# Kernel optimization log

Measured on AMD Instinct MI355X. Metric: run time of the kernel, lower is better.

## Reference

```python
import jax, jax.numpy as jnp
import numpy as np

N = 20000   # nodes
E = 640000  # edges (avg degree 32)
D = 128     # input_nf == output_nf
H = 128     # hidden_size


def silu(x):
    return x * jax.nn.sigmoid(x)


def setup_inputs() -> dict:
    key = jax.random.key(0)
    ks = jax.random.split(key, 16)
    def lin(k, out_d, in_d, scale=None):
        s = scale if scale is not None else (1.0 / np.sqrt(in_d))
        return jax.random.uniform(k, (out_d, in_d), jnp.float32, -s, s)
    return {
        "h": jax.random.normal(ks[0], (N, D), jnp.float32),
        "coord": jax.random.normal(ks[1], (N, 3), jnp.float32),
        "edge_index": jax.random.randint(ks[2], (2, E), 0, N, jnp.int32),
        # edge_mlp: Linear(2D+1 -> H), Linear(H -> H)
        "We1": lin(ks[3], H, 2 * D + 1), "be1": jnp.zeros((H,), jnp.float32),
        "We2": lin(ks[4], H, H),          "be2": jnp.zeros((H,), jnp.float32),
        # node_mlp: Linear(H+D -> H), Linear(H -> D)
        "Wn1": lin(ks[5], H, H + D),      "bn1": jnp.zeros((H,), jnp.float32),
        "Wn2": lin(ks[6], D, H),          "bn2": jnp.zeros((D,), jnp.float32),
        # coord_mlp: Linear(H -> H), Linear(H -> 1, no bias, xavier gain=0.001)
        "Wc1": lin(ks[7], H, H),          "bc1": jnp.zeros((H,), jnp.float32),
        "Wc2": lin(ks[8], 1, H, scale=0.001 * np.sqrt(6.0 / (H + 1))),
    }


def reference(h, coord, edge_index, We1, be1, We2, be2, Wn1, bn1, Wn2, bn2, Wc1, bc1, Wc2):
    src, dst = edge_index[0], edge_index[1]

    # coord2radial (normalize=False)
    coord_diff = coord[src] - coord[dst]                 # [E, 3]
    radial = jnp.sum(coord_diff * coord_diff, axis=1, keepdims=True)  # [E, 1]

    # edge model: cat(h[src], h[dst], radial) -> Lin -> SiLU -> Lin -> SiLU
    e_in = jnp.concatenate([h[src], h[dst], radial], axis=1)  # [E, 2D+1]
    edge_feat = silu(silu(e_in @ We1.T + be1) @ We2.T + be2)  # [E, H]

    # coord model: coord_diff * coord_mlp(edge_feat), scatter-add over src
    w = silu(edge_feat @ Wc1.T + bc1) @ Wc2.T                 # [E, 1]
    trans = coord_diff * w                                    # [E, 3]
    coord_out = coord + jax.ops.segment_sum(trans, src, num_segments=N)

    # node model: agg edge_feat over src, cat(h, agg) -> Lin -> SiLU -> Lin, residual
    agg = jax.ops.segment_sum(edge_feat, src, num_segments=N)  # [N, H]
    n_in = jnp.concatenate([h, agg], axis=1)                   # [N, H+D]
    h_out = h + (silu(n_in @ Wn1.T + bn1) @ Wn2.T + bn2)       # [N, D]

    return (h_out, coord_out)
```

## Files before the change

kernel.cpp:

```cpp
#include <hip/hip_runtime.h>

#define N_NODES 20000
#define N_EDGES 640000
#define D 128
#define H 128

#define EB    128
#define TPB   512
#define NBLK2 512
#define NTILE (N_EDGES / EB)
#define EBN   64
#define NNT64 ((N_NODES + EBN - 1) / EBN)
#define ST    136

#define WS_W1   0
#define WS_W2   65536
#define WS_WC1  98304
#define WS_WN1  131072
#define WS_WN2  196608
#define WS_CNT  229376
#define WS_CUR  309376
#define WS_PERM 389376
#define WS_U    2949376
#define WS_V    8069376
#define WS_P    13189376

typedef short bf16x8 __attribute__((ext_vector_type(8)));
typedef float f32x4  __attribute__((ext_vector_type(4)));

__device__ __forceinline__ float silu_f(float x) {
    return x * __builtin_amdgcn_rcpf(1.0f + __expf(-x));
}
__device__ __forceinline__ ushort f2b(float f) {
    union { float f; unsigned int u; } v; v.f = f;
    return (ushort)((v.u + 0x7FFF + ((v.u >> 16) & 1)) >> 16);
}
__device__ __forceinline__ float b2f(ushort s) {
    union { unsigned int u; float f; } v; v.u = ((unsigned int)s) << 16; return v.f;
}
__device__ __forceinline__ unsigned f2b2(float lo, float hi) {
    unsigned r;
    asm("v_cvt_pk_bf16_f32 %0, %1, %2" : "=v"(r) : "v"(lo), "v"(hi));
    return r;
}

__device__ __forceinline__ void bar_lds() {
    asm volatile("s_waitcnt lgkmcnt(0)" ::: "memory");
    __builtin_amdgcn_s_barrier();
    asm volatile("" ::: "memory");
}

__device__ __forceinline__ void gemm_chunk_rw(const ushort* Ab, int kc0,
                                              const bf16x8 b[2], f32x4 acc[4][2],
                                              int eg, int lane)
{
    const int r = lane & 15, g = lane >> 4;
    bf16x8 a[4];
    #pragma unroll
    for (int mt = 0; mt < 4; ++mt)
        a[mt] = *(const bf16x8*)&Ab[(eg * 64 + mt * 16 + r) * ST + kc0 + g * 8];
    #pragma unroll
    for (int mt = 0; mt < 4; ++mt)
        #pragma unroll
        for (int nt = 0; nt < 2; ++nt)
            acc[mt][nt] = __builtin_amdgcn_mfma_f32_16x16x32_bf16(a[mt], b[nt], acc[mt][nt], 0, 0, 0);
}

__device__ __forceinline__ void zero_acc8(f32x4 acc[4][2]) {
    #pragma unroll
    for (int mt = 0; mt < 4; ++mt)
        #pragma unroll
        for (int nt = 0; nt < 2; ++nt)
            acc[mt][nt] = (f32x4){0.f, 0.f, 0.f, 0.f};
}

__device__ __forceinline__ void epi_silu8(f32x4 acc[4][2], const float* bias,
                                          ushort* out, int eg, int cg, int lane) {
    const int r = lane & 15, g = lane >> 4;
    #pragma unroll
    for (int nt = 0; nt < 2; ++nt) {
        int o = cg * 32 + nt * 16 + r;
        float bo = bias[o];
        #pragma unroll
        for (int mt = 0; mt < 4; ++mt)
            #pragma unroll
            for (int j = 0; j < 4; ++j) {
                int e = eg * 64 + mt * 16 + g * 4 + j;
                out[e * ST + o] = f2b(silu_f(acc[mt][nt][j] + bo));
            }
    }
}

__device__ __forceinline__ void epi_silu8_pk(f32x4 acc[4][2], const float* bias,
                                             ushort* out, int eg, int cg, int lane) {
    const int r = lane & 15, g = lane >> 4;
    #pragma unroll
    for (int nt = 0; nt < 2; ++nt) {
        int o = cg * 32 + nt * 16 + r;
        float bo = bias[o];
        #pragma unroll
        for (int mt = 0; mt < 4; ++mt) {
            int e = eg * 64 + mt * 16 + g * 4;
            unsigned p01 = f2b2(silu_f(acc[mt][nt][0] + bo), silu_f(acc[mt][nt][1] + bo));
            unsigned p23 = f2b2(silu_f(acc[mt][nt][2] + bo), silu_f(acc[mt][nt][3] + bo));
            out[(e + 0) * ST + o] = (ushort)p01;
            out[(e + 1) * ST + o] = (ushort)(p01 >> 16);
            out[(e + 2) * ST + o] = (ushort)p23;
            out[(e + 3) * ST + o] = (ushort)(p23 >> 16);
        }
    }
}

__global__ void prep2(const float* __restrict__ We1, const float* __restrict__ We2,
                      const float* __restrict__ Wc1, const float* __restrict__ Wn1,
                      const float* __restrict__ Wn2, const float* __restrict__ coordp,
                      const int* __restrict__ eidx,
                      ushort* w1, ushort* w2, ushort* wc1, ushort* wn1, ushort* wn2,
                      float* cout, int* cnt)
{
    int idx = blockIdx.x * 256 + threadIdx.x;
    if (idx < N_EDGES) atomicAdd(&cnt[eidx[idx]], 1);
    int j = idx;
    if (j < 32768) { w1[j] = f2b(We1[(j >> 8) * 257 + (j & 255)]); return; }
    j -= 32768;
    if (j < 16384) { w2[j] = f2b(We2[j]); return; }
    j -= 16384;
    if (j < 16384) { wc1[j] = f2b(Wc1[j]); return; }
    j -= 16384;
    if (j < 32768) { wn1[j] = f2b(Wn1[j]); return; }
    j -= 32768;
    if (j < 16384) { wn2[j] = f2b(Wn2[j]); return; }
    j -= 16384;
    if (j < N_NODES * 3) cout[j] = coordp[j];
}

__global__ __launch_bounds__(256, 2)
void uvp_k(const float* __restrict__ h,
           const ushort* __restrict__ w1b, const ushort* __restrict__ wn1b,
           const float* __restrict__ be1, const float* __restrict__ bn1,
           ushort* __restrict__ u, ushort* __restrict__ v, ushort* __restrict__ p)
{
    __shared__ __align__(16) ushort hs[EBN * ST];
    __shared__ float b1s[H], bn1s[H];

    const int tid = threadIdx.x, lane = tid & 63, wv = tid >> 6;
    const int eg = wv >> 2, cg = wv & 3;
    const int r = lane & 15, g = lane >> 4;
    const int n0 = blockIdx.x * EBN;

    if (tid < 128) b1s[tid] = be1[tid];
    else if (tid < 256) bn1s[tid - 128] = bn1[tid - 128];

    bf16x8 wa[4][2], wb[4][2], wn[4][2];
    {
        const int c0 = cg * 32 + r, c1c = c0 + 16;
        #pragma unroll
        for (int kc = 0; kc < 4; ++kc) {
            wa[kc][0] = *(const bf16x8*)&w1b [c0  * 256 +       kc * 32 + g * 8];
            wa[kc][1] = *(const bf16x8*)&w1b [c1c * 256 +       kc * 32 + g * 8];
            wb[kc][0] = *(const bf16x8*)&w1b [c0  * 256 + 128 + kc * 32 + g * 8];
            wb[kc][1] = *(const bf16x8*)&w1b [c1c * 256 + 128 + kc * 32 + g * 8];
            wn[kc][0] = *(const bf16x8*)&wn1b[c0  * 256 +       kc * 32 + g * 8];
            wn[kc][1] = *(const bf16x8*)&wn1b[c1c * 256 +       kc * 32 + g * 8];
        }
    }
    #pragma unroll
    for (int it = 0; it < 8; ++it) {
        int idx = tid + it * 256;
        int e = idx >> 5, c = idx & 31;
        int n = n0 + e; if (n >= N_NODES) n = 0;
        float4 vv = *(const float4*)&h[(size_t)n * D + c * 4];
        ushort4 pk; pk.x = f2b(vv.x); pk.y = f2b(vv.y); pk.z = f2b(vv.z); pk.w = f2b(vv.w);
        *(ushort4*)&hs[e * ST + c * 4] = pk;
    }
    __syncthreads();

    f32x4 acc[4][2];
    zero_acc8(acc);
    #pragma unroll
    for (int kc = 0; kc < 4; ++kc) gemm_chunk_rw(hs, kc * 32, wa[kc], acc, eg, lane);
    #pragma unroll
    for (int nt = 0; nt < 2; ++nt) {
        int o = cg * 32 + nt * 16 + r;
        float bo = b1s[o];
        #pragma unroll
        for (int mt = 0; mt < 4; ++mt)
            #pragma unroll
            for (int j = 0; j < 4; ++j) {
                int n = n0 + eg * 64 + mt * 16 + g * 4 + j;
                if (n < N_NODES) u[(size_t)n * H + o] = f2b(acc[mt][nt][j] + bo);
            }
    }
    zero_acc8(acc);
    #pragma unroll
    for (int kc = 0; kc < 4; ++kc) gemm_chunk_rw(hs, kc * 32, wb[kc], acc, eg, lane);
    #pragma unroll
    for (int nt = 0; nt < 2; ++nt) {
        int o = cg * 32 + nt * 16 + r;
        #pragma unroll
        for (int mt = 0; mt < 4; ++mt)
            #pragma unroll
            for (int j = 0; j < 4; ++j) {
                int n = n0 + eg * 64 + mt * 16 + g * 4 + j;
                if (n < N_NODES) v[(size_t)n * H + o] = f2b(acc[mt][nt][j]);
            }
    }
    zero_acc8(acc);
    #pragma unroll
    for (int kc = 0; kc < 4; ++kc) gemm_chunk_rw(hs, kc * 32, wn[kc], acc, eg, lane);
    #pragma unroll
    for (int nt = 0; nt < 2; ++nt) {
        int o = cg * 32 + nt * 16 + r;
        float bo = bn1s[o];
        #pragma unroll
        for (int mt = 0; mt < 4; ++mt)
            #pragma unroll
            for (int j = 0; j < 4; ++j) {
                int n = n0 + eg * 64 + mt * 16 + g * 4 + j;
                if (n < N_NODES) p[(size_t)n * H + o] = f2b(acc[mt][nt][j] + bo);
            }
    }
}

__global__ void scan_k(const int* __restrict__ cnt, int* cur) {
    __shared__ int wsum[16];
    __shared__ int carry_s;
    const int t = threadIdx.x, lane = t & 63, wid = t >> 6;
    if (t == 0) carry_s = 0;
    __syncthreads();
    for (int base = 0; base < N_NODES; base += 1024) {
        int i = base + t;
        int vv = (i < N_NODES) ? cnt[i] : 0;
        int s = vv;
        #pragma unroll
        for (int d = 1; d < 64; d <<= 1) {
            int x = __shfl_up(s, d);
            if (lane >= d) s += x;
        }
        if (lane == 63) wsum[wid] = s;
        __syncthreads();
        if (wid == 0) {
            int ws = (lane < 16) ? wsum[lane] : 0;
            #pragma unroll
            for (int d = 1; d < 16; d <<= 1) {
                int x = __shfl_up(ws, d);
                if (lane >= d) ws += x;
            }
            if (lane < 16) wsum[lane] = ws;
        }
        __syncthreads();
        int woff = (wid > 0) ? wsum[wid - 1] : 0;
        if (i < N_NODES) cur[i] = carry_s + woff + s - vv;
        __syncthreads();
        if (t == 0) carry_s += wsum[15];
        __syncthreads();
    }
}

__global__ void scatter_k(const int* __restrict__ eidx, int* cur, int* perm) {
    int e = blockIdx.x * 256 + threadIdx.x;
    if (e < N_EDGES) {
        int pp = atomicAdd(&cur[eidx[e]], 1);
        perm[pp] = e;
    }
}

__global__ __launch_bounds__(TPB, 2)
void egcl_edge(const ushort* __restrict__ u, const ushort* __restrict__ v,
               const int* __restrict__ eidx, const int* __restrict__ perm,
               const float* __restrict__ coordp,
               const ushort* __restrict__ w2b, const ushort* __restrict__ wc1b,
               const float* __restrict__ We1,
               const float* __restrict__ be2, const float* __restrict__ bc1,
               const float* __restrict__ Wc2,
               float* __restrict__ agg, float* __restrict__ coord_out)
{
    __shared__ __align__(16) ushort t1[EB * ST];
    __shared__ __align__(16) ushort ef[EB * ST];
    __shared__ int   srcs_s[2][EB], dsts_s[2][EB];
    __shared__ float radial_s[2][EB];
    __shared__ float cdx_s[2][EB], cdy_s[2][EB], cdz_s[2][EB];
    __shared__ float wcop[4][EB];
    __shared__ float b2s[H], bc1s[H], wc2s[H], w256s[H];

    const int tid = threadIdx.x, lane = tid & 63, wv = tid >> 6;
    const int eg = wv >> 2, cg = wv & 3;
    const int r = lane & 15, g = lane >> 4;
    const int ce = tid >> 2, cq = tid & 3;

    if (tid < 128)      b2s[tid] = be2[tid];
    else if (tid < 256) bc1s[tid - 128] = bc1[tid - 128];
    else if (tid < 384) wc2s[tid - 256] = Wc2[tid - 256];
    else                w256s[tid - 384] = We1[(tid - 384) * 257 + 256];

    bf16x8 w2f[4][2], w3f[4][2];
    {
        const int c0 = cg * 32 + r, c1c = c0 + 16;
        #pragma unroll
        for (int kc = 0; kc < 4; ++kc) {
            w2f[kc][0] = *(const bf16x8*)&w2b [c0  * 128 + kc * 32 + g * 8];
            w2f[kc][1] = *(const bf16x8*)&w2b [c1c * 128 + kc * 32 + g * 8];
            w3f[kc][0] = *(const bf16x8*)&wc1b[c0  * 128 + kc * 32 + g * 8];
            w3f[kc][1] = *(const bf16x8*)&wc1b[c1c * 128 + kc * 32 + g * 8];
        }
    }

    int t = (int)blockIdx.x;
    int rs = 0, rd = 0;
    float rsx = 0, rsy = 0, rsz = 0, rdx = 0, rdy = 0, rdz = 0;
    if (tid < EB) {
        int e = perm[t * EB + tid];
        int s = eidx[e], d = eidx[N_EDGES + e];
        srcs_s[0][tid] = s; dsts_s[0][tid] = d;
        float sx = coordp[s * 3], sy = coordp[s * 3 + 1], sz = coordp[s * 3 + 2];
        float dx0 = coordp[d * 3], dy0 = coordp[d * 3 + 1], dz0 = coordp[d * 3 + 2];
        float dx = sx - dx0, dy = sy - dy0, dz = sz - dz0;
        cdx_s[0][tid] = dx; cdy_s[0][tid] = dy; cdz_s[0][tid] = dz;
        radial_s[0][tid] = dx * dx + dy * dy + dz * dz;
    }
    __syncthreads();

    bf16x8 uvr[8];
    {
        const ushort* up = u + (size_t)srcs_s[0][ce] * H + cq * 32;
        const ushort* vp = v + (size_t)dsts_s[0][ce] * H + cq * 32;
        #pragma unroll
        for (int i = 0; i < 4; ++i) {
            uvr[i]     = *(const bf16x8*)(up + i * 8);
            uvr[4 + i] = *(const bf16x8*)(vp + i * 8);
        }
    }
    if (tid < EB && t + NBLK2 < NTILE) {
        int e = perm[(t + NBLK2) * EB + tid];
        rs = eidx[e]; rd = eidx[N_EDGES + e];
        rsx = coordp[rs * 3]; rsy = coordp[rs * 3 + 1]; rsz = coordp[rs * 3 + 2];
        rdx = coordp[rd * 3]; rdy = coordp[rd * 3 + 1]; rdz = coordp[rd * 3 + 2];
    }

    f32x4 acc[4][2];
    int pb = 0;

    for (; t < NTILE; t += NBLK2) {
        {
            float rad = radial_s[pb][ce];
            #pragma unroll
            for (int i = 0; i < 4; ++i) {
                float4 wlo = *(const float4*)&w256s[cq * 32 + i * 8];
                float4 whi = *(const float4*)&w256s[cq * 32 + i * 8 + 4];
                bf16x8 uu = uvr[i], vx = uvr[4 + i];
                float x0 = silu_f(b2f((ushort)uu[0]) + b2f((ushort)vx[0]) + rad * wlo.x);
                float x1 = silu_f(b2f((ushort)uu[1]) + b2f((ushort)vx[1]) + rad * wlo.y);
                float x2 = silu_f(b2f((ushort)uu[2]) + b2f((ushort)vx[2]) + rad * wlo.z);
                float x3 = silu_f(b2f((ushort)uu[3]) + b2f((ushort)vx[3]) + rad * wlo.w);
                float x4 = silu_f(b2f((ushort)uu[4]) + b2f((ushort)vx[4]) + rad * whi.x);
                float x5 = silu_f(b2f((ushort)uu[5]) + b2f((ushort)vx[5]) + rad * whi.y);
                float x6 = silu_f(b2f((ushort)uu[6]) + b2f((ushort)vx[6]) + rad * whi.z);
                float x7 = silu_f(b2f((ushort)uu[7]) + b2f((ushort)vx[7]) + rad * whi.w);
                uint4 pk4;
                pk4.x = f2b2(x0, x1); pk4.y = f2b2(x2, x3);
                pk4.z = f2b2(x4, x5); pk4.w = f2b2(x6, x7);
                *(uint4*)&t1[ce * ST + cq * 32 + i * 8] = pk4;
            }
        }
        if (tid < EB) {
            srcs_s[pb ^ 1][tid] = rs; dsts_s[pb ^ 1][tid] = rd;
            float dx = rsx - rdx, dy = rsy - rdy, dz = rsz - rdz;
            cdx_s[pb ^ 1][tid] = dx; cdy_s[pb ^ 1][tid] = dy; cdz_s[pb ^ 1][tid] = dz;
            radial_s[pb ^ 1][tid] = dx * dx + dy * dy + dz * dz;
        }
        bar_lds();

        int en = 0;
        if (tid < EB && t + 2 * NBLK2 < NTILE) en = perm[(t + 2 * NBLK2) * EB + tid];
        zero_acc8(acc);
        __builtin_amdgcn_s_setprio(1);
        #pragma unroll
        for (int kc = 0; kc < 4; ++kc) gemm_chunk_rw(t1, kc * 32, w2f[kc], acc, eg, lane);
        __builtin_amdgcn_s_setprio(0);
        epi_silu8_pk(acc, b2s, ef, eg, cg, lane);
        bar_lds();

        {
            const ushort* up = u + (size_t)srcs_s[pb ^ 1][ce] * H + cq * 32;
            const ushort* vp = v + (size_t)dsts_s[pb ^ 1][ce] * H + cq * 32;
            #pragma unroll
            for (int i = 0; i < 4; ++i) {
                uvr[i]     = *(const bf16x8*)(up + i * 8);
                uvr[4 + i] = *(const bf16x8*)(vp + i * 8);
            }
        }
        int rs2 = 0, rd2 = 0;
        if (tid < EB) { rs2 = eidx[en]; rd2 = eidx[N_EDGES + en]; }
        {
            f32x4 acc3[2][4];
            #pragma unroll
            for (int ot = 0; ot < 2; ++ot)
                #pragma unroll
                for (int et = 0; et < 4; ++et)
                    acc3[ot][et] = (f32x4){0.f, 0.f, 0.f, 0.f};
            __builtin_amdgcn_s_setprio(1);
            #pragma unroll
            for (int kc = 0; kc < 4; ++kc) {
                bf16x8 bfr[4];
                #pragma unroll
                for (int et = 0; et < 4; ++et)
                    bfr[et] = *(const bf16x8*)&ef[(eg * 64 + et * 16 + r) * ST + kc * 32 + g * 8];
                #pragma unroll
                for (int ot = 0; ot < 2; ++ot)
                    #pragma unroll
                    for (int et = 0; et < 4; ++et)
                        acc3[ot][et] = __builtin_amdgcn_mfma_f32_16x16x32_bf16(
                            w3f[kc][ot], bfr[et], acc3[ot][et], 0, 0, 0);
            }
            __builtin_amdgcn_s_setprio(0);
            float partial[4] = {0.f, 0.f, 0.f, 0.f};
            #pragma unroll
            for (int ot = 0; ot < 2; ++ot) {
                int ob = cg * 32 + ot * 16 + g * 4;
                float4 wq = *(const float4*)&wc2s[ob];
                float4 bq = *(const float4*)&bc1s[ob];
                #pragma unroll
                for (int et = 0; et < 4; ++et) {
                    partial[et] += silu_f(acc3[ot][et][0] + bq.x) * wq.x
                                 + silu_f(acc3[ot][et][1] + bq.y) * wq.y
                                 + silu_f(acc3[ot][et][2] + bq.z) * wq.z
                                 + silu_f(acc3[ot][et][3] + bq.w) * wq.w;
                }
            }
            #pragma unroll
            for (int et = 0; et < 4; ++et) {
                float s_ = partial[et];
                s_ += __shfl_xor(s_, 16);
                s_ += __shfl_xor(s_, 32);
                if (g == 0) wcop[cg][eg * 64 + et * 16 + r] = s_;
            }
        }
        {
            int o = tid & 127, q = tid >> 7;
            int base = q * 32;
            float sum = 0.f;
            int curs = srcs_s[pb][base];
            for (int k = 0; k < 32; ++k) {
                int e = base + k;
                int s = srcs_s[pb][e];
                if (s != curs) {
                    atomicAdd(&agg[(size_t)curs * D + o], sum);
                    sum = 0.f; curs = s;
                }
                sum += b2f(ef[e * ST + o]);
            }
            atomicAdd(&agg[(size_t)curs * D + o], sum);
        }
        bar_lds();

        if (tid < EB) {
            rs = rs2; rd = rd2;
            rsx = coordp[rs * 3]; rsy = coordp[rs * 3 + 1]; rsz = coordp[rs * 3 + 2];
            rdx = coordp[rd * 3]; rdy = coordp[rd * 3 + 1]; rdz = coordp[rd * 3 + 2];
        }
        {
            float s_ = wcop[cq][ce];
            s_ += __shfl_down(s_, 2);
            s_ += __shfl_down(s_, 1);
            float wfull = __shfl(s_, lane & ~3);
            if (cq < 3) {
                float cdv = (cq == 0) ? cdx_s[pb][ce] : (cq == 1) ? cdy_s[pb][ce] : cdz_s[pb][ce];
                atomicAdd(&coord_out[(size_t)srcs_s[pb][ce] * 3 + cq], cdv * wfull);
            }
        }
        bar_lds();
        pb ^= 1;
    }
}

__global__ __launch_bounds__(256, 4)
void egcl_node(const float* __restrict__ h,
               const ushort* __restrict__ wn1b, const ushort* __restrict__ wn2b,
               const ushort* __restrict__ pArr, const float* __restrict__ bn2,
               float* __restrict__ hout )
{
    __shared__ __align__(16) ushort t1[EBN * ST];
    __shared__ __align__(16) ushort t2[EBN * ST];
    __shared__ float b2s[H];

    const int tid = threadIdx.x, lane = tid & 63, wv = tid >> 6;
    const int eg = wv >> 2, cg = wv & 3;
    const int r = lane & 15, g = lane >> 4;
    const int n0 = blockIdx.x * EBN;

    if (tid < 128) b2s[tid] = bn2[tid];

    bf16x8 wnb[4][2], w2f[4][2];
    {
        const int c0 = cg * 32 + r, c1c = c0 + 16;
        #pragma unroll
        for (int kc = 0; kc < 4; ++kc) {
            wnb[kc][0] = *(const bf16x8*)&wn1b[c0  * 256 + 128 + kc * 32 + g * 8];
            wnb[kc][1] = *(const bf16x8*)&wn1b[c1c * 256 + 128 + kc * 32 + g * 8];
            w2f[kc][0] = *(const bf16x8*)&wn2b[c0  * 128 + kc * 32 + g * 8];
            w2f[kc][1] = *(const bf16x8*)&wn2b[c1c * 128 + kc * 32 + g * 8];
        }
    }
    #pragma unroll
    for (int it = 0; it < 8; ++it) {
        int idx = tid + it * 256;
        int e = idx >> 5, c = idx & 31;
        int n = n0 + e; if (n >= N_NODES) n = 0;
        float4 vv = *(const float4*)&hout[(size_t)n * D + c * 4];
        ushort4 pk; pk.x = f2b(vv.x); pk.y = f2b(vv.y); pk.z = f2b(vv.z); pk.w = f2b(vv.w);
        *(ushort4*)&t1[e * ST + c * 4] = pk;
    }
    __syncthreads();

    f32x4 acc[4][2];
    zero_acc8(acc);
    #pragma unroll
    for (int kc = 0; kc < 4; ++kc) gemm_chunk_rw(t1, kc * 32, wnb[kc], acc, eg, lane);
    #pragma unroll
    for (int nt = 0; nt < 2; ++nt) {
        int o = cg * 32 + nt * 16 + r;
        #pragma unroll
        for (int mt = 0; mt < 4; ++mt)
            #pragma unroll
            for (int j = 0; j < 4; ++j) {
                int e = eg * 64 + mt * 16 + g * 4 + j;
                int n = n0 + e; if (n >= N_NODES) n = 0;
                float x = acc[mt][nt][j] + b2f(pArr[(size_t)n * H + o]);
                t2[e * ST + o] = f2b(silu_f(x));
            }
    }
    __syncthreads();

    zero_acc8(acc);
    #pragma unroll
    for (int kc = 0; kc < 4; ++kc) gemm_chunk_rw(t2, kc * 32, w2f[kc], acc, eg, lane);
    #pragma unroll
    for (int nt = 0; nt < 2; ++nt) {
        int o = cg * 32 + nt * 16 + r;
        float bo = b2s[o];
        #pragma unroll
        for (int mt = 0; mt < 4; ++mt)
            #pragma unroll
            for (int j = 0; j < 4; ++j) {
                int n = n0 + eg * 64 + mt * 16 + g * 4 + j;
                if (n < N_NODES)
                    hout[(size_t)n * D + o] = h[(size_t)n * D + o] + acc[mt][nt][j] + bo;
            }
    }
}

extern "C" void kernel_launch(void* const* d_in, const int* in_sizes, int n_in,
                              void* d_out, int out_size, void* d_ws, size_t ws_size,
                              hipStream_t stream)
{
    const float* h     = (const float*)d_in[0];
    const float* coord = (const float*)d_in[1];
    const int*   eidx  = (const int*)d_in[2];
    const float* We1 = (const float*)d_in[3];
    const float* be1 = (const float*)d_in[4];
    const float* We2 = (const float*)d_in[5];
    const float* be2 = (const float*)d_in[6];
    const float* Wn1 = (const float*)d_in[7];
    const float* bn1 = (const float*)d_in[8];
    const float* Wn2 = (const float*)d_in[9];
    const float* bn2 = (const float*)d_in[10];
    const float* Wc1 = (const float*)d_in[11];
    const float* bc1 = (const float*)d_in[12];
    const float* Wc2 = (const float*)d_in[13];

    float* hout = (float*)d_out;
    float* cout = (float*)d_out + (size_t)N_NODES * D;

    char* ws = (char*)d_ws;
    ushort* w1b  = (ushort*)(ws + WS_W1);
    ushort* w2b  = (ushort*)(ws + WS_W2);
    ushort* wc1b = (ushort*)(ws + WS_WC1);
    ushort* wn1b = (ushort*)(ws + WS_WN1);
    ushort* wn2b = (ushort*)(ws + WS_WN2);
    int* cnt  = (int*)(ws + WS_CNT);
    int* cur  = (int*)(ws + WS_CUR);
    int* perm = (int*)(ws + WS_PERM);
    ushort* uArr = (ushort*)(ws + WS_U);
    ushort* vArr = (ushort*)(ws + WS_V);
    ushort* pArr = (ushort*)(ws + WS_P);

    hipMemsetAsync(hout, 0, (size_t)N_NODES * D * sizeof(float), stream);
    hipMemsetAsync(cnt, 0, N_NODES * sizeof(int), stream);
    prep2<<<(N_EDGES + 255) / 256, 256, 0, stream>>>(We1, We2, Wc1, Wn1, Wn2, coord, eidx,
                                                     w1b, w2b, wc1b, wn1b, wn2b, cout, cnt);
    scan_k<<<1, 1024, 0, stream>>>(cnt, cur);
    scatter_k<<<(N_EDGES + 255) / 256, 256, 0, stream>>>(eidx, cur, perm);
    uvp_k<<<NNT64, 256, 0, stream>>>(h, w1b, wn1b, be1, bn1, uArr, vArr, pArr);
    egcl_edge<<<NBLK2, TPB, 0, stream>>>(uArr, vArr, eidx, perm, coord,
                                         w2b, wc1b, We1, be2, bc1, Wc2,
                                         hout, cout);
    egcl_node<<<NNT64, 256, 0, stream>>>(h, wn1b, wn2b, pArr, bn2, hout);
}
```

Before: 319.7 us.

## Fuse scan into prep via last-block pattern, merge scatter into uvp, drop barrier

The separate single-block scan kernel is folded into prep2: the last block to finish, detected by an atomic counter, does the prefix scan. The edge-permutation scatter becomes extra blocks of the uvp kernel, which removes two launches and their serialization. In egcl_edge, the per-edge coord weight is reduced with shuffles and atomically added straight to coord_out, so the wcop LDS buffer and one barrier per tile go away. In exchange, coord_out takes more atomics because each column group adds its own partial, and the serial scan now runs as the tail of prep2.

```diff
diff --git a/kernel.cpp b/kernel.cpp
--- a/kernel.cpp
+++ b/kernel.cpp
@@ -11,6 +11,7 @@
 #define NTILE (N_EDGES / EB)
 #define EBN   64
 #define NNT64 ((N_NODES + EBN - 1) / EBN)
+#define NSCAT ((N_EDGES + 255) / 256)
 #define ST    136
 
 #define WS_W1   0
@@ -111,39 +112,88 @@
     }
 }
 
-__global__ void prep2(const float* __restrict__ We1, const float* __restrict__ We2,
-                      const float* __restrict__ Wc1, const float* __restrict__ Wn1,
-                      const float* __restrict__ Wn2, const float* __restrict__ coordp,
-                      const int* __restrict__ eidx,
-                      ushort* w1, ushort* w2, ushort* wc1, ushort* wn1, ushort* wn2,
-                      float* cout, int* cnt)
+__global__ __launch_bounds__(1024)
+void prep2(const float* __restrict__ We1, const float* __restrict__ We2,
+           const float* __restrict__ Wc1, const float* __restrict__ Wn1,
+           const float* __restrict__ Wn2, const float* __restrict__ coordp,
+           const int* __restrict__ eidx,
+           ushort* w1, ushort* w2, ushort* wc1, ushort* wn1, ushort* wn2,
+           float* cout, int* cnt, int* cur)
 {
-    int idx = blockIdx.x * 256 + threadIdx.x;
+    const int tid = threadIdx.x;
+    int idx = blockIdx.x * 1024 + tid;
     if (idx < N_EDGES) atomicAdd(&cnt[eidx[idx]], 1);
     int j = idx;
-    if (j < 32768) { w1[j] = f2b(We1[(j >> 8) * 257 + (j & 255)]); return; }
-    j -= 32768;
-    if (j < 16384) { w2[j] = f2b(We2[j]); return; }
-    j -= 16384;
-    if (j < 16384) { wc1[j] = f2b(Wc1[j]); return; }
-    j -= 16384;
-    if (j < 32768) { wn1[j] = f2b(Wn1[j]); return; }
-    j -= 32768;
-    if (j < 16384) { wn2[j] = f2b(Wn2[j]); return; }
-    j -= 16384;
-    if (j < N_NODES * 3) cout[j] = coordp[j];
+    if (j < 32768) { w1[j] = f2b(We1[(j >> 8) * 257 + (j & 255)]); }
+    else if ((j -= 32768) < 16384) { w2[j] = f2b(We2[j]); }
+    else if ((j -= 16384) < 16384) { wc1[j] = f2b(Wc1[j]); }
+    else if ((j -= 16384) < 32768) { wn1[j] = f2b(Wn1[j]); }
+    else if ((j -= 32768) < 16384) { wn2[j] = f2b(Wn2[j]); }
+    else if ((j -= 16384) < N_NODES * 3) { cout[j] = coordp[j]; }
+
+    __shared__ int lastFlag;
+    __shared__ int wsum[16];
+    __shared__ int carry_s;
+    __threadfence();
+    __syncthreads();
+    if (tid == 0) lastFlag = (atomicAdd(&cnt[N_NODES], 1) == (int)gridDim.x - 1);
+    __syncthreads();
+    if (!lastFlag) return;
+    __threadfence();
+    const int lane = tid & 63, wid = tid >> 6;
+    if (tid == 0) carry_s = 0;
+    __syncthreads();
+    for (int base = 0; base < N_NODES; base += 1024) {
+        int i = base + tid;
+        int vv = 0;
+        if (i < N_NODES)
+            vv = __hip_atomic_load(&cnt[i], __ATOMIC_RELAXED, __HIP_MEMORY_SCOPE_AGENT);
+        int s = vv;
+        #pragma unroll
+        for (int d = 1; d < 64; d <<= 1) {
+            int x = __shfl_up(s, d);
+            if (lane >= d) s += x;
+        }
+        if (lane == 63) wsum[wid] = s;
+        __syncthreads();
+        if (wid == 0) {
+            int ws = (lane < 16) ? wsum[lane] : 0;
+            #pragma unroll
+            for (int d = 1; d < 16; d <<= 1) {
+                int x = __shfl_up(ws, d);
+                if (lane >= d) ws += x;
+            }
+            if (lane < 16) wsum[lane] = ws;
+        }
+        __syncthreads();
+        int woff = (wid > 0) ? wsum[wid - 1] : 0;
+        if (i < N_NODES) cur[i] = carry_s + woff + s - vv;
+        __syncthreads();
+        if (tid == 0) carry_s += wsum[15];
+        __syncthreads();
+    }
 }
 
 __global__ __launch_bounds__(256, 2)
-void uvp_k(const float* __restrict__ h,
-           const ushort* __restrict__ w1b, const ushort* __restrict__ wn1b,
-           const float* __restrict__ be1, const float* __restrict__ bn1,
-           ushort* __restrict__ u, ushort* __restrict__ v, ushort* __restrict__ p)
+void uvp_scatter_k(const float* __restrict__ h,
+                   const ushort* __restrict__ w1b, const ushort* __restrict__ wn1b,
+                   const float* __restrict__ be1, const float* __restrict__ bn1,
+                   ushort* __restrict__ u, ushort* __restrict__ v, ushort* __restrict__ p,
+                   const int* __restrict__ eidx, int* cur, int* perm)
 {
+    const int tid = threadIdx.x;
+    if (blockIdx.x >= NNT64) {
+        int e = (blockIdx.x - NNT64) * 256 + tid;
+        if (e < N_EDGES) {
+            int pp = atomicAdd(&cur[eidx[e]], 1);
+            perm[pp] = e;
+        }
+        return;
+    }
     __shared__ __align__(16) ushort hs[EBN * ST];
     __shared__ float b1s[H], bn1s[H];
 
-    const int tid = threadIdx.x, lane = tid & 63, wv = tid >> 6;
+    const int lane = tid & 63, wv = tid >> 6;
     const int eg = wv >> 2, cg = wv & 3;
     const int r = lane & 15, g = lane >> 4;
     const int n0 = blockIdx.x * EBN;
@@ -219,49 +269,6 @@
                 int n = n0 + eg * 64 + mt * 16 + g * 4 + j;
                 if (n < N_NODES) p[(size_t)n * H + o] = f2b(acc[mt][nt][j] + bo);
             }
-    }
-}
-
-__global__ void scan_k(const int* __restrict__ cnt, int* cur) {
-    __shared__ int wsum[16];
-    __shared__ int carry_s;
-    const int t = threadIdx.x, lane = t & 63, wid = t >> 6;
-    if (t == 0) carry_s = 0;
-    __syncthreads();
-    for (int base = 0; base < N_NODES; base += 1024) {
-        int i = base + t;
-        int vv = (i < N_NODES) ? cnt[i] : 0;
-        int s = vv;
-        #pragma unroll
-        for (int d = 1; d < 64; d <<= 1) {
-            int x = __shfl_up(s, d);
-            if (lane >= d) s += x;
-        }
-        if (lane == 63) wsum[wid] = s;
-        __syncthreads();
-        if (wid == 0) {
-            int ws = (lane < 16) ? wsum[lane] : 0;
-            #pragma unroll
-            for (int d = 1; d < 16; d <<= 1) {
-                int x = __shfl_up(ws, d);
-                if (lane >= d) ws += x;
-            }
-            if (lane < 16) wsum[lane] = ws;
-        }
-        __syncthreads();
-        int woff = (wid > 0) ? wsum[wid - 1] : 0;
-        if (i < N_NODES) cur[i] = carry_s + woff + s - vv;
-        __syncthreads();
-        if (t == 0) carry_s += wsum[15];
-        __syncthreads();
-    }
-}
-
-__global__ void scatter_k(const int* __restrict__ eidx, int* cur, int* perm) {
-    int e = blockIdx.x * 256 + threadIdx.x;
-    if (e < N_EDGES) {
-        int pp = atomicAdd(&cur[eidx[e]], 1);
-        perm[pp] = e;
     }
 }
 
@@ -280,7 +287,6 @@
     __shared__ int   srcs_s[2][EB], dsts_s[2][EB];
     __shared__ float radial_s[2][EB];
     __shared__ float cdx_s[2][EB], cdy_s[2][EB], cdz_s[2][EB];
-    __shared__ float wcop[4][EB];
     __shared__ float b2s[H], bc1s[H], wc2s[H], w256s[H];
 
     const int tid = threadIdx.x, lane = tid & 63, wv = tid >> 6;
@@ -427,13 +433,21 @@
                                  + silu_f(acc3[ot][et][3] + bq.w) * wq.w;
                 }
             }
+            const float* cdp = (g == 0) ? cdx_s[pb] : (g == 1) ? cdy_s[pb] : cdz_s[pb];
             #pragma unroll
             for (int et = 0; et < 4; ++et) {
                 float s_ = partial[et];
                 s_ += __shfl_xor(s_, 16);
                 s_ += __shfl_xor(s_, 32);
-                if (g == 0) wcop[cg][eg * 64 + et * 16 + r] = s_;
-            }
+                int e = eg * 64 + et * 16 + r;
+                if (g < 3)
+                    atomicAdd(&coord_out[(size_t)srcs_s[pb][e] * 3 + g], cdp[e] * s_);
+            }
+        }
+        if (tid < EB) {
+            rs = rs2; rd = rd2;
+            rsx = coordp[rs * 3]; rsy = coordp[rs * 3 + 1]; rsz = coordp[rs * 3 + 2];
+            rdx = coordp[rd * 3]; rdy = coordp[rd * 3 + 1]; rdz = coordp[rd * 3 + 2];
         }
         {
             int o = tid & 127, q = tid >> 7;
@@ -450,23 +464,6 @@
                 sum += b2f(ef[e * ST + o]);
             }
             atomicAdd(&agg[(size_t)curs * D + o], sum);
-        }
-        bar_lds();
-
-        if (tid < EB) {
-            rs = rs2; rd = rd2;
-            rsx = coordp[rs * 3]; rsy = coordp[rs * 3 + 1]; rsz = coordp[rs * 3 + 2];
-            rdx = coordp[rd * 3]; rdy = coordp[rd * 3 + 1]; rdz = coordp[rd * 3 + 2];
-        }
-        {
-            float s_ = wcop[cq][ce];
-            s_ += __shfl_down(s_, 2);
-            s_ += __shfl_down(s_, 1);
-            float wfull = __shfl(s_, lane & ~3);
-            if (cq < 3) {
-                float cdv = (cq == 0) ? cdx_s[pb][ce] : (cq == 1) ? cdy_s[pb][ce] : cdz_s[pb][ce];
-                atomicAdd(&coord_out[(size_t)srcs_s[pb][ce] * 3 + cq], cdv * wfull);
-            }
         }
         bar_lds();
         pb ^= 1;
@@ -585,12 +582,12 @@
     ushort* pArr = (ushort*)(ws + WS_P);
 
     hipMemsetAsync(hout, 0, (size_t)N_NODES * D * sizeof(float), stream);
-    hipMemsetAsync(cnt, 0, N_NODES * sizeof(int), stream);
-    prep2<<<(N_EDGES + 255) / 256, 256, 0, stream>>>(We1, We2, Wc1, Wn1, Wn2, coord, eidx,
-                                                     w1b, w2b, wc1b, wn1b, wn2b, cout, cnt);
-    scan_k<<<1, 1024, 0, stream>>>(cnt, cur);
-    scatter_k<<<(N_EDGES + 255) / 256, 256, 0, stream>>>(eidx, cur, perm);
-    uvp_k<<<NNT64, 256, 0, stream>>>(h, w1b, wn1b, be1, bn1, uArr, vArr, pArr);
+    hipMemsetAsync(cnt, 0, (N_NODES + 1) * sizeof(int), stream);
+    prep2<<<(N_EDGES + 1023) / 1024, 1024, 0, stream>>>(
+        We1, We2, Wc1, Wn1, Wn2, coord, eidx,
+        w1b, w2b, wc1b, wn1b, wn2b, cout, cnt, cur);
+    uvp_scatter_k<<<NNT64 + NSCAT, 256, 0, stream>>>(
+        h, w1b, wn1b, be1, bn1, uArr, vArr, pArr, eidx, cur, perm);
     egcl_edge<<<NBLK2, TPB, 0, stream>>>(uArr, vArr, eidx, perm, coord,
                                          w2b, wc1b, We1, be2, bc1, Wc2,
                                          hout, cout);
```

After: 1.010 ms. 3.16x slower.
